# Kernel optimization log

Hardware: AMD Instinct MI355X
Metric: run time of the kernel (lower is better)

## Reference

```python
import jax, jax.numpy as jnp
import numpy as np

B, L, H, M, E, NH, R = 4, 512, 1024, 128, 64, 16, 1024   # docs, seq, hidden, mentions, entities, heads, pairs
D, BLK, C = 768, 64, 97                                   # embed_size, block_size, num_class


def setup_inputs() -> dict:
    key = jax.random.key(0)
    ks = jax.random.split(key, 9)
    seq_lhs = jax.random.normal(ks[0], (B, L, H), jnp.float32)
    ent_lhs = jax.random.normal(ks[1], (B, M, H), jnp.float32)
    ent_to_seq_attn = jax.random.uniform(ks[2], (B, NH, M, L), jnp.float32)
    entity_id_labels = jax.random.randint(ks[3], (B, M), 0, E, jnp.int32)
    hts = jax.random.randint(ks[4], (B, R, 2), 0, E, jnp.int32)
    Wh = jax.random.normal(ks[5], (2 * H, D), jnp.float32) * 0.02
    Wt = jax.random.normal(ks[6], (2 * H, D), jnp.float32) * 0.02
    Wb = jax.random.normal(ks[7], (D * BLK, C), jnp.float32) * 0.02
    return dict(seq_lhs=seq_lhs, ent_lhs=ent_lhs, ent_to_seq_attn=ent_to_seq_attn,
                entity_id_labels=entity_id_labels, hts=hts,
                Wh=Wh, bh=jnp.zeros((D,), jnp.float32),
                Wt=Wt, bt=jnp.zeros((D,), jnp.float32),
                Wb=Wb, bb=jnp.zeros((C,), jnp.float32))


def reference(seq_lhs, ent_lhs, ent_to_seq_attn, entity_id_labels, hts, Wh, bh, Wt, bt, Wb, bb):
    # --- hrt_pool: segment logsumexp / mean over mentions per entity ---
    mask = entity_id_labels[:, None, :] == jnp.arange(E, dtype=entity_id_labels.dtype)[None, :, None]  # [B,E,M]
    cnt = mask.sum(-1)  # [B,E]
    neg = jnp.asarray(-1e30, ent_lhs.dtype)
    masked = jnp.where(mask[..., None], ent_lhs[:, None, :, :], neg)          # [B,E,M,H]
    lse = jax.nn.logsumexp(masked, axis=2)                                    # [B,E,H]
    ent_emb = jnp.where((cnt > 0)[..., None], lse, 0.0)
    mf = mask.astype(ent_to_seq_attn.dtype)
    attn_sum = jnp.einsum('bem,bhml->behl', mf, ent_to_seq_attn)              # [B,E,NH,L]
    denom = jnp.maximum(cnt, 1).astype(attn_sum.dtype)[..., None, None]
    ent_attn = jnp.where((cnt > 0)[..., None, None], attn_sum / denom, 0.0)
    # --- gather head/tail entities per pair ---
    h_idx, t_idx = hts[..., 0], hts[..., 1]                                   # [B,R]
    hs = jnp.take_along_axis(ent_emb, h_idx[..., None], axis=1)               # [B,R,H]
    ts = jnp.take_along_axis(ent_emb, t_idx[..., None], axis=1)
    h_attn = jnp.take_along_axis(ent_attn, h_idx[..., None, None], axis=1)    # [B,R,NH,L]
    t_attn = jnp.take_along_axis(ent_attn, t_idx[..., None, None], axis=1)
    ht_attn = (h_attn * t_attn).mean(axis=2)                                  # [B,R,L]
    ht_attn = ht_attn / (ht_attn.sum(-1, keepdims=True) + 1e-5)
    rel = jnp.einsum('brl,bld->brd', ht_attn, seq_lhs)                        # [B,R,H]
    # --- extractors + block bilinear ---
    hcat = jnp.concatenate([hs, rel], -1).reshape(B * R, 2 * H)
    tcat = jnp.concatenate([ts, rel], -1).reshape(B * R, 2 * H)
    hv = jnp.tanh(hcat @ Wh + bh)
    tv = jnp.tanh(tcat @ Wt + bt)
    b1 = hv.reshape(-1, D // BLK, BLK)
    b2 = tv.reshape(-1, D // BLK, BLK)
    bl = (b1[:, :, :, None] * b2[:, :, None, :]).reshape(-1, D * BLK)
    return bl @ Wb + bb                                                       # [B*R, C]
```

## Files before the change

### kernel.cpp

```cpp
#include <hip/hip_runtime.h>
#include <hip/hip_bf16.h>
#include <math.h>

#define B_  4
#define L_  512
#define H_  1024
#define M_  128
#define E_  64
#define NH_ 16
#define R_  1024
#define D_  768
#define BLK_ 64
#define C_  97
#define NROW (B_*R_)
#define KB_  (D_/BLK_)

typedef __attribute__((ext_vector_type(8))) unsigned short ushort8;
typedef __attribute__((ext_vector_type(4))) unsigned short ushort4v;
typedef __attribute__((ext_vector_type(8))) short s8;
typedef __attribute__((ext_vector_type(4))) float f4;

__device__ __forceinline__ unsigned short f2bf(float x) {
    unsigned u = __builtin_bit_cast(unsigned, x);
    unsigned r = (u + 0x7fffu + ((u >> 16) & 1u)) >> 16;
    return (unsigned short)r;
}
__device__ __forceinline__ float bf2f(unsigned short h) {
    unsigned u = ((unsigned)h) << 16;
    return __builtin_bit_cast(float, u);
}
__device__ __forceinline__ float lo16f(unsigned u) { return __builtin_bit_cast(float, u << 16); }
__device__ __forceinline__ float hi16f(unsigned u) { return __builtin_bit_cast(float, u & 0xffff0000u); }

__device__ __forceinline__ void gload_lds16(const unsigned short* g, unsigned short* l)
{
    __builtin_amdgcn_global_load_lds(
        (const __attribute__((address_space(1))) unsigned int*)g,
        (__attribute__((address_space(3))) unsigned int*)l, 16, 0, 0);
}

__global__ __launch_bounds__(256) void pool_lse(
    const float* __restrict__ ent_lhs, const int* __restrict__ labels,
    unsigned short* __restrict__ ent_embB)
{
    int be = blockIdx.x, b = be >> 6, e = be & 63;
    __shared__ int midx[M_];
    __shared__ int scnt;
    if (threadIdx.x == 0) scnt = 0;
    __syncthreads();
    if (threadIdx.x < M_) {
        if (labels[b*M_ + threadIdx.x] == e) {
            int p = atomicAdd(&scnt, 1);
            midx[p] = threadIdx.x;
        }
    }
    __syncthreads();
    int cnt = scnt;
    for (int h = threadIdx.x; h < H_; h += blockDim.x) {
        float r = 0.f;
        if (cnt > 0) {
            const float* base = ent_lhs + (size_t)b*M_*H_ + h;
            float mx = -INFINITY;
            for (int k = 0; k < cnt; ++k) mx = fmaxf(mx, base[(size_t)midx[k]*H_]);
            float s = 0.f;
            for (int k = 0; k < cnt; ++k) s += expf(base[(size_t)midx[k]*H_] - mx);
            r = mx + logf(s);
        }
        ent_embB[(size_t)be*H_ + h] = f2bf(r);
    }
}

__global__ __launch_bounds__(256) void pool_attn(
    const float* __restrict__ attn, const int* __restrict__ labels,
    unsigned short* __restrict__ ent_attnB)
{
    int e  = blockIdx.x;
    int y  = blockIdx.y;
    int b  = y >> 4, nh = y & 15;
    __shared__ int midx[M_];
    __shared__ int scnt;
    if (threadIdx.x == 0) scnt = 0;
    __syncthreads();
    if (threadIdx.x < M_) {
        if (labels[b*M_ + threadIdx.x] == e) {
            int p = atomicAdd(&scnt, 1);
            midx[p] = threadIdx.x;
        }
    }
    __syncthreads();
    int cnt = scnt;
    float inv = (cnt > 0) ? 1.f/(float)cnt : 0.f;
    const float* base = attn + ((size_t)(b*NH_ + nh)*M_)*L_;
    #pragma unroll
    for (int q = 0; q < 2; ++q) {
        int l = threadIdx.x + q*256;
        float s = 0.f;
        for (int k = 0; k < cnt; ++k) s += base[(size_t)midx[k]*L_ + l];
        ent_attnB[((size_t)(b*E_ + e)*NH_ + nh)*L_ + l] = f2bf(s * inv);
    }
}

__global__ __launch_bounds__(256) void pair_attn_kernel(
    const unsigned short* __restrict__ entA, const int* __restrict__ hts,
    unsigned short* __restrict__ htA)
{
    int w  = threadIdx.x >> 6, ln = threadIdx.x & 63;
    int br = blockIdx.x*4 + w, b = br >> 10;
    int hi = hts[br*2 + 0], ti = hts[br*2 + 1];
    const unsigned* ph = (const unsigned*)(entA + ((size_t)(b*E_ + hi)*NH_)*L_);
    const unsigned* pt = (const unsigned*)(entA + ((size_t)(b*E_ + ti)*NH_)*L_);
    float v0[4] = {0.f, 0.f, 0.f, 0.f};
    float v1[4] = {0.f, 0.f, 0.f, 0.f};
    #pragma unroll
    for (int nh = 0; nh < NH_; ++nh) {
        #pragma unroll
        for (int c = 0; c < 4; ++c) {
            int l2 = ln + c*64;
            unsigned a = ph[nh*(L_/2) + l2], d = pt[nh*(L_/2) + l2];
            v0[c] += lo16f(a)*lo16f(d);
            v1[c] += hi16f(a)*hi16f(d);
        }
    }
    float part = 0.f;
    #pragma unroll
    for (int c = 0; c < 4; ++c) part += v0[c] + v1[c];
    #pragma unroll
    for (int off = 32; off > 0; off >>= 1) part += __shfl_xor(part, off, 64);
    float norm = 1.f / (part*(1.f/16.f) + 1e-5f);
    #pragma unroll
    for (int c = 0; c < 4; ++c) {
        unsigned short o0 = f2bf(v0[c]*(1.f/16.f)*norm);
        unsigned short o1 = f2bf(v1[c]*(1.f/16.f)*norm);
        *(unsigned*)(htA + (size_t)br*L_ + (size_t)(ln + c*64)*2) = ((unsigned)o1 << 16) | o0;
    }
}

__global__ __launch_bounds__(256) void transpose_cvt_seq(const float* __restrict__ in,
                                                         unsigned short* __restrict__ outp)
{
    int b = blockIdx.z;
    int h0 = blockIdx.x*32, l0 = blockIdx.y*32;
    __shared__ float tile[32][33];
    int tx = threadIdx.x & 31, ty = threadIdx.x >> 5;
    #pragma unroll
    for (int p = 0; p < 4; ++p)
        tile[ty + p*8][tx] = in[((size_t)b*L_ + l0 + ty + p*8)*H_ + h0 + tx];
    __syncthreads();
    #pragma unroll
    for (int p = 0; p < 4; ++p)
        outp[((size_t)b*H_ + h0 + ty + p*8)*L_ + l0 + tx] = f2bf(tile[tx][ty + p*8]);
}

__global__ __launch_bounds__(256) void transpose_cvt_W(const float* __restrict__ Wh,
                                                       const float* __restrict__ Wt,
                                                       unsigned short* __restrict__ WhT,
                                                       unsigned short* __restrict__ WtT)
{
    const float* in = blockIdx.z ? Wt : Wh;
    unsigned short* outp = blockIdx.z ? WtT : WhT;
    int n0 = blockIdx.x*32, k0 = blockIdx.y*32;
    __shared__ float tile[32][33];
    int tx = threadIdx.x & 31, ty = threadIdx.x >> 5;
    #pragma unroll
    for (int p = 0; p < 4; ++p)
        tile[ty + p*8][tx] = in[((size_t)(k0 + ty + p*8))*D_ + n0 + tx];
    __syncthreads();
    #pragma unroll
    for (int p = 0; p < 4; ++p) {
        int n = n0 + ty + p*8;
        outp[(size_t)n*2048 + k0 + tx] = f2bf(tile[tx][ty + p*8]);
    }
}

__global__ __launch_bounds__(256) void prep_gather(const unsigned short* __restrict__ entE,
                                                   const int* __restrict__ hts,
                                                   unsigned short* __restrict__ Ah,
                                                   unsigned short* __restrict__ At)
{
    int n = blockIdx.x, b = n >> 10;
    int m = threadIdx.x >> 7, off = (threadIdx.x & 127)*8;
    int idx = hts[n*2 + m];
    const unsigned short* src = entE + (size_t)(b*E_ + idx)*H_ + off;
    unsigned short* dst = (m ? At : Ah) + (size_t)n*2048 + off;
    *(ushort8*)dst = *(const ushort8*)src;
}

__global__ __launch_bounds__(256) void prep_WbT(const float* __restrict__ Wb,
                                                unsigned short* __restrict__ outp)
{
    int blk = blockIdx.x;
    __shared__ float sW[64*97];
    const float* src = Wb + (size_t)blk*64*97;
    for (int e = threadIdx.x; e < 64*97; e += 256) sW[e] = src[e];
    __syncthreads();
    unsigned short* dst = outp + (size_t)blk*128*64;
    for (int e = threadIdx.x; e < 128*64; e += 256) {
        int wcq = e >> 12;
        int ct  = (e >> 10) & 3;
        int j2  = (e >> 9) & 1;
        int qd  = (e >> 7) & 3;
        int lm  = (e >> 3) & 15;
        int t   = e & 7;
        int c   = wcq*64 + ct*16 + lm;
        int j   = j2*32 + qd*8 + t;
        dst[e] = (c < C_) ? f2bf(sW[j*97 + c]) : (unsigned short)0;
    }
}

__device__ __forceinline__ void gemm128_core(const unsigned short* __restrict__ A,
                                             const unsigned short* __restrict__ Bt,
                                             int K, int row0, int col0,
                                             f4 (&acc)[4][4])
{
    __shared__ __attribute__((aligned(16))) unsigned short As[128][32];
    __shared__ __attribute__((aligned(16))) unsigned short Bs[128][32];
    int tid = threadIdx.x;
    int wave = tid >> 6, lane = tid & 63;
    int wr = wave & 1, wc = wave >> 1;
    int lm = lane & 15, quad = lane >> 4;

    for (int k0 = 0; k0 < K; k0 += 32) {
        #pragma unroll
        for (int s = 0; s < 2; ++s) {
            int ch = tid + s*256;
            int row = ch >> 2, part = ch & 3;
            gload_lds16(A  + (size_t)(row0 + row)*K + k0 + part*8, &As[0][0] + ch*8);
            gload_lds16(Bt + (size_t)(col0 + row)*K + k0 + part*8, &Bs[0][0] + ch*8);
        }
        __syncthreads();
        s8 a[4], b[4];
        #pragma unroll
        for (int ti = 0; ti < 4; ++ti) a[ti] = *(const s8*)&As[wr*64 + ti*16 + lm][quad*8];
        #pragma unroll
        for (int tj = 0; tj < 4; ++tj) b[tj] = *(const s8*)&Bs[wc*64 + tj*16 + lm][quad*8];
        #pragma unroll
        for (int ti = 0; ti < 4; ++ti)
            #pragma unroll
            for (int tj = 0; tj < 4; ++tj)
                acc[ti][tj] = __builtin_amdgcn_mfma_f32_16x16x32_bf16(a[ti], b[tj], acc[ti][tj], 0, 0, 0);
        __syncthreads();
    }
}

__global__ __launch_bounds__(256) void gemm_rel_mfma(const unsigned short* __restrict__ htA,
                                                     const unsigned short* __restrict__ seqT,
                                                     unsigned short* __restrict__ Ah,
                                                     unsigned short* __restrict__ At)
{
    int z = blockIdx.z;
    const unsigned short* A  = htA  + (size_t)z*R_*L_;
    const unsigned short* Bt = seqT + (size_t)z*H_*L_;
    int row0 = blockIdx.y*128, col0 = blockIdx.x*128;
    f4 acc[4][4] = {};
    gemm128_core(A, Bt, L_, row0, col0, acc);
    int lane = threadIdx.x & 63, wave = threadIdx.x >> 6;
    int wr = wave & 1, wc = wave >> 1, lm = lane & 15, quad = lane >> 4;
    #pragma unroll
    for (int ti = 0; ti < 4; ++ti)
        #pragma unroll
        for (int tj = 0; tj < 4; ++tj)
            #pragma unroll
            for (int r = 0; r < 4; ++r) {
                int n   = z*R_ + row0 + wr*64 + ti*16 + quad*4 + r;
                int col = col0 + wc*64 + tj*16 + lm;
                unsigned short v = f2bf(acc[ti][tj][r]);
                Ah[(size_t)n*2048 + 1024 + col] = v;
                At[(size_t)n*2048 + 1024 + col] = v;
            }
}

__global__ __launch_bounds__(256) void gemm_ext_mfma(
    const unsigned short* __restrict__ Ah, const unsigned short* __restrict__ At,
    const unsigned short* __restrict__ WhT, const unsigned short* __restrict__ WtT,
    const float* __restrict__ bh, const float* __restrict__ bt,
    float* __restrict__ hv, float* __restrict__ tv)
{
    int z = blockIdx.z;
    const unsigned short* A  = z ? At  : Ah;
    const unsigned short* Bt = z ? WtT : WhT;
    const float* bias = z ? bt : bh;
    float* C = z ? tv : hv;
    int row0 = blockIdx.y*128, col0 = blockIdx.x*128;
    f4 acc[4][4] = {};
    gemm128_core(A, Bt, 2048, row0, col0, acc);
    int lane = threadIdx.x & 63, wave = threadIdx.x >> 6;
    int wr = wave & 1, wc = wave >> 1, lm = lane & 15, quad = lane >> 4;
    #pragma unroll
    for (int ti = 0; ti < 4; ++ti)
        #pragma unroll
        for (int tj = 0; tj < 4; ++tj)
            #pragma unroll
            for (int r = 0; r < 4; ++r) {
                int row = row0 + wr*64 + ti*16 + quad*4 + r;
                int col = col0 + wc*64 + tj*16 + lm;
                float x = acc[ti][tj][r] + bias[col];
                float e = __expf(2.f*x);
                C[(size_t)row*D_ + col] = 1.f - 2.f/(e + 1.f);
            }
}

__global__ void out_init(const float* __restrict__ bb, float* __restrict__ out)
{
    int i = blockIdx.x*256 + threadIdx.x;
    if (i < NROW*C_) out[i] = bb[i % C_];
}

__device__ __forceinline__ void loadB_frag(const unsigned short* __restrict__ bbase,
                                           int i, s8 (&dst)[4][2])
{
    #pragma unroll
    for (int ct = 0; ct < 4; ++ct) {
        dst[ct][0] = *(const s8*)(bbase + (size_t)i*8192 + ct*1024);
        dst[ct][1] = *(const s8*)(bbase + (size_t)i*8192 + ct*1024 + 512);
    }
}

__device__ __forceinline__ void compute_i4(const s8 (&bfr)[4][2],
                                           const float (&sh)[4],
                                           const float (&tvv)[4][2][8],
                                           f4 (&acc)[4][4])
{
    s8 afr[4][2];
    #pragma unroll
    for (int rt = 0; rt < 4; ++rt)
        #pragma unroll
        for (int j2 = 0; j2 < 2; ++j2) {
            union { unsigned u[4]; s8 v; } cv;
            #pragma unroll
            for (int t2 = 0; t2 < 4; ++t2) {
                float pe = sh[rt] * tvv[rt][j2][t2*2];
                float po = sh[rt] * tvv[rt][j2][t2*2 + 1];
                cv.u[t2] = __builtin_amdgcn_perm(__builtin_bit_cast(unsigned, po),
                                                 __builtin_bit_cast(unsigned, pe),
                                                 0x07060302u);
            }
            afr[rt][j2] = cv.v;
        }
    #pragma unroll
    for (int ct = 0; ct < 4; ++ct)
        #pragma unroll
        for (int rt = 0; rt < 4; ++rt) {
            acc[rt][ct] = __builtin_amdgcn_mfma_f32_16x16x32_bf16(afr[rt][0], bfr[ct][0], acc[rt][ct], 0, 0, 0);
            acc[rt][ct] = __builtin_amdgcn_mfma_f32_16x16x32_bf16(afr[rt][1], bfr[ct][1], acc[rt][ct], 0, 0, 0);
        }
}

__global__ __launch_bounds__(256) void final_mfma(
    const float* __restrict__ hv,
    const float* __restrict__ tv,
    const unsigned short* __restrict__ WbT,
    float* __restrict__ out)
{
    int kb   = blockIdx.x;
    int row0 = blockIdx.y * 128;
    __shared__ __attribute__((aligned(16))) unsigned short hS[128][72];
    __shared__ __attribute__((aligned(16))) unsigned short tS[128][72];

    int tid = threadIdx.x;
    for (int e = tid; e < 2048; e += 256) {
        int r = e >> 4, part = e & 15;
        float4 xh = *(const float4*)(hv + (size_t)(row0 + r)*D_ + kb*BLK_ + part*4);
        float4 xt = *(const float4*)(tv + (size_t)(row0 + r)*D_ + kb*BLK_ + part*4);
        ushort4v ph = { f2bf(xh.x), f2bf(xh.y), f2bf(xh.z), f2bf(xh.w) };
        ushort4v pt = { f2bf(xt.x), f2bf(xt.y), f2bf(xt.z), f2bf(xt.w) };
        *(ushort4v*)&hS[r][part*4] = ph;
        *(ushort4v*)&tS[r][part*4] = pt;
    }
    int wave = tid >> 6, lane = tid & 63;
    int wr = wave & 1, wc = wave >> 1;
    int lm = lane & 15, quad = lane >> 4;
    __syncthreads();

    float tvv[4][2][8];
    #pragma unroll
    for (int rt = 0; rt < 4; ++rt)
        #pragma unroll
        for (int j2 = 0; j2 < 2; ++j2) {
            int r = wr*64 + rt*16 + lm;
            ushort8 w = *(const ushort8*)&tS[r][j2*32 + quad*8];
            #pragma unroll
            for (int t = 0; t < 8; ++t) tvv[rt][j2][t] = bf2f(w[t]);
        }

    f4 acc[4][4] = {};
    const unsigned short* bbase = WbT + (size_t)kb*(64*128*64)
                                + (size_t)wc*4096 + ((size_t)quad*16 + lm)*8;

    s8 bufA[4][2], bufB[4][2];
    loadB_frag(bbase, 0, bufA);
    for (int i0 = 0; i0 < 64; i0 += 2) {
        loadB_frag(bbase, i0 + 1, bufB);
        {
            float sh[4];
            #pragma unroll
            for (int rt = 0; rt < 4; ++rt) sh[rt] = bf2f(hS[wr*64 + rt*16 + lm][i0]);
            compute_i4(bufA, sh, tvv, acc);
        }
        if (i0 < 62) loadB_frag(bbase, i0 + 2, bufA);
        {
            float sh[4];
            #pragma unroll
            for (int rt = 0; rt < 4; ++rt) sh[rt] = bf2f(hS[wr*64 + rt*16 + lm][i0 + 1]);
            compute_i4(bufB, sh, tvv, acc);
        }
    }

    #pragma unroll
    for (int rt = 0; rt < 4; ++rt)
        #pragma unroll
        for (int ct = 0; ct < 4; ++ct)
            #pragma unroll
            for (int r = 0; r < 4; ++r) {
                int row = row0 + wr*64 + rt*16 + quad*4 + r;
                int col = wc*64 + ct*16 + lm;
                if (col < C_) atomicAdd(out + (size_t)row*C_ + col, acc[rt][ct][r]);
            }
}

extern "C" void kernel_launch(void* const* d_in, const int* in_sizes, int n_in,
                              void* d_out, int out_size, void* d_ws, size_t ws_size,
                              hipStream_t stream)
{
    const float* seq_lhs = (const float*)d_in[0];
    const float* ent_lhs = (const float*)d_in[1];
    const float* attn    = (const float*)d_in[2];
    const int*   labels  = (const int*)d_in[3];
    const int*   hts     = (const int*)d_in[4];
    const float* Wh      = (const float*)d_in[5];
    const float* bh      = (const float*)d_in[6];
    const float* Wt      = (const float*)d_in[7];
    const float* bt      = (const float*)d_in[8];
    const float* Wb      = (const float*)d_in[9];
    const float* bb      = (const float*)d_in[10];
    float* out = (float*)d_out;

    float* wsf      = (float*)d_ws;
    float* hv       = wsf;
    float* tv       = hv + 3145728;
    unsigned short* ent_embB  = (unsigned short*)(tv + 3145728);
    unsigned short* ent_attnB = ent_embB  + 262144;
    unsigned short* htA       = ent_attnB + 2097152;
    unsigned short* seqT      = htA       + 2097152;
    unsigned short* WhT       = seqT      + 2097152;
    unsigned short* WtT       = WhT       + 1572864;
    unsigned short* Ah        = WtT       + 1572864;
    unsigned short* At        = Ah        + 8388608;
    unsigned short* WbT       = At        + 8388608;

    transpose_cvt_W<<<dim3(24, 64, 2), 256, 0, stream>>>(Wh, Wt, WhT, WtT);
    prep_WbT<<<KB_*64, 256, 0, stream>>>(Wb, WbT);
    transpose_cvt_seq<<<dim3(32, 16, B_), 256, 0, stream>>>(seq_lhs, seqT);

    pool_lse<<<B_*E_, 256, 0, stream>>>(ent_lhs, labels, ent_embB);
    pool_attn<<<dim3(E_, B_*NH_), 256, 0, stream>>>(attn, labels, ent_attnB);
    pair_attn_kernel<<<B_*R_/4, 256, 0, stream>>>(ent_attnB, hts, htA);
    gemm_rel_mfma<<<dim3(8, 8, B_), 256, 0, stream>>>(htA, seqT, Ah, At);
    prep_gather<<<NROW, 256, 0, stream>>>(ent_embB, hts, Ah, At);
    gemm_ext_mfma<<<dim3(6, 32, 2), 256, 0, stream>>>(Ah, At, WhT, WtT, bh, bt, hv, tv);
    out_init<<<(NROW*C_ + 255)/256, 256, 0, stream>>>(bb, out);
    final_mfma<<<dim3(KB_, NROW/128), 256, 0, stream>>>(hv, tv, WbT, out);
}
```

Before: 300.4 us.

## Precompute entity projections once and split extractor GEMM to skip gathered half

Splits the concatenated extractor GEMM algebraically. The entity-embedding half is now computed once per entity (256 rows, split-K with atomicAdd into bias-initialized buffers) rather than once per pair (4096 rows). The per-pair GEMM now only covers the rel half (K=1024), adding the gathered entity projection in the epilogue. This removes the prep_gather kernel, the duplicated rel writes into Ah/At, and half of the largest GEMM's FLOPs, at the cost of fp32 atomics and an extra small GEMM launch.

```diff
diff --git a/kernel.cpp b/kernel.cpp
--- a/kernel.cpp
+++ b/kernel.cpp
@@ -172,19 +172,6 @@
     }
 }
 
-__global__ __launch_bounds__(256) void prep_gather(const unsigned short* __restrict__ entE,
-                                                   const int* __restrict__ hts,
-                                                   unsigned short* __restrict__ Ah,
-                                                   unsigned short* __restrict__ At)
-{
-    int n = blockIdx.x, b = n >> 10;
-    int m = threadIdx.x >> 7, off = (threadIdx.x & 127)*8;
-    int idx = hts[n*2 + m];
-    const unsigned short* src = entE + (size_t)(b*E_ + idx)*H_ + off;
-    unsigned short* dst = (m ? At : Ah) + (size_t)n*2048 + off;
-    *(ushort8*)dst = *(const ushort8*)src;
-}
-
 __global__ __launch_bounds__(256) void prep_WbT(const float* __restrict__ Wb,
                                                 unsigned short* __restrict__ outp)
 {
@@ -207,8 +194,8 @@
     }
 }
 
-__device__ __forceinline__ void gemm128_core(const unsigned short* __restrict__ A,
-                                             const unsigned short* __restrict__ Bt,
+__device__ __forceinline__ void gemm128_core(const unsigned short* __restrict__ A, int lda,
+                                             const unsigned short* __restrict__ Bt, int ldb,
                                              int K, int row0, int col0,
                                              f4 (&acc)[4][4])
 {
@@ -224,8 +211,8 @@
         for (int s = 0; s < 2; ++s) {
             int ch = tid + s*256;
             int row = ch >> 2, part = ch & 3;
-            gload_lds16(A  + (size_t)(row0 + row)*K + k0 + part*8, &As[0][0] + ch*8);
-            gload_lds16(Bt + (size_t)(col0 + row)*K + k0 + part*8, &Bs[0][0] + ch*8);
+            gload_lds16(A  + (size_t)(row0 + row)*lda + k0 + part*8, &As[0][0] + ch*8);
+            gload_lds16(Bt + (size_t)(col0 + row)*ldb + k0 + part*8, &Bs[0][0] + ch*8);
         }
         __syncthreads();
         s8 a[4], b[4];
@@ -244,15 +231,14 @@
 
 __global__ __launch_bounds__(256) void gemm_rel_mfma(const unsigned short* __restrict__ htA,
                                                      const unsigned short* __restrict__ seqT,
-                                                     unsigned short* __restrict__ Ah,
-                                                     unsigned short* __restrict__ At)
+                                                     unsigned short* __restrict__ relB)
 {
     int z = blockIdx.z;
     const unsigned short* A  = htA  + (size_t)z*R_*L_;
     const unsigned short* Bt = seqT + (size_t)z*H_*L_;
     int row0 = blockIdx.y*128, col0 = blockIdx.x*128;
     f4 acc[4][4] = {};
-    gemm128_core(A, Bt, L_, row0, col0, acc);
+    gemm128_core(A, L_, Bt, L_, L_, row0, col0, acc);
     int lane = threadIdx.x & 63, wave = threadIdx.x >> 6;
     int wr = wave & 1, wc = wave >> 1, lm = lane & 15, quad = lane >> 4;
     #pragma unroll
@@ -263,26 +249,22 @@
             for (int r = 0; r < 4; ++r) {
                 int n   = z*R_ + row0 + wr*64 + ti*16 + quad*4 + r;
                 int col = col0 + wc*64 + tj*16 + lm;
-                unsigned short v = f2bf(acc[ti][tj][r]);
-                Ah[(size_t)n*2048 + 1024 + col] = v;
-                At[(size_t)n*2048 + 1024 + col] = v;
+                relB[(size_t)n*H_ + col] = f2bf(acc[ti][tj][r]);
             }
 }
 
-__global__ __launch_bounds__(256) void gemm_ext_mfma(
-    const unsigned short* __restrict__ Ah, const unsigned short* __restrict__ At,
+__global__ __launch_bounds__(256) void gemm_p_mfma(
+    const unsigned short* __restrict__ ent_embB,
     const unsigned short* __restrict__ WhT, const unsigned short* __restrict__ WtT,
-    const float* __restrict__ bh, const float* __restrict__ bt,
-    float* __restrict__ hv, float* __restrict__ tv)
+    float* __restrict__ Ph, float* __restrict__ Pt)
 {
     int z = blockIdx.z;
-    const unsigned short* A  = z ? At  : Ah;
     const unsigned short* Bt = z ? WtT : WhT;
-    const float* bias = z ? bt : bh;
-    float* C = z ? tv : hv;
-    int row0 = blockIdx.y*128, col0 = blockIdx.x*128;
+    float* P = z ? Pt : Ph;
+    int mt = blockIdx.y & 1, ks = blockIdx.y >> 1;
+    int row0 = mt*128, col0 = blockIdx.x*128;
     f4 acc[4][4] = {};
-    gemm128_core(A, Bt, 2048, row0, col0, acc);
+    gemm128_core(ent_embB + ks*256, H_, Bt + ks*256, 2048, 256, row0, col0, acc);
     int lane = threadIdx.x & 63, wave = threadIdx.x >> 6;
     int wr = wave & 1, wc = wave >> 1, lm = lane & 15, quad = lane >> 4;
     #pragma unroll
@@ -293,16 +275,55 @@
             for (int r = 0; r < 4; ++r) {
                 int row = row0 + wr*64 + ti*16 + quad*4 + r;
                 int col = col0 + wc*64 + tj*16 + lm;
-                float x = acc[ti][tj][r] + bias[col];
+                atomicAdd(P + (size_t)row*D_ + col, acc[ti][tj][r]);
+            }
+}
+
+__global__ __launch_bounds__(256) void gemm_ext_mfma(
+    const unsigned short* __restrict__ relB,
+    const unsigned short* __restrict__ WhT, const unsigned short* __restrict__ WtT,
+    const float* __restrict__ Ph, const float* __restrict__ Pt,
+    const int* __restrict__ hts,
+    float* __restrict__ hv, float* __restrict__ tv)
+{
+    int z = blockIdx.z;
+    const unsigned short* Bt = (z ? WtT : WhT) + 1024;
+    const float* P = z ? Pt : Ph;
+    float* Cv = z ? tv : hv;
+    int row0 = blockIdx.y*128, col0 = blockIdx.x*128;
+    f4 acc[4][4] = {};
+    gemm128_core(relB, H_, Bt, 2048, H_, row0, col0, acc);
+    int lane = threadIdx.x & 63, wave = threadIdx.x >> 6;
+    int wr = wave & 1, wc = wave >> 1, lm = lane & 15, quad = lane >> 4;
+    #pragma unroll
+    for (int ti = 0; ti < 4; ++ti)
+        #pragma unroll
+        for (int r = 0; r < 4; ++r) {
+            int row = row0 + wr*64 + ti*16 + quad*4 + r;
+            int b   = row >> 10;
+            int idx = hts[row*2 + z];
+            const float* prow = P + ((size_t)(b*E_ + idx))*D_;
+            #pragma unroll
+            for (int tj = 0; tj < 4; ++tj) {
+                int col = col0 + wc*64 + tj*16 + lm;
+                float x = acc[ti][tj][r] + prow[col];
                 float e = __expf(2.f*x);
-                C[(size_t)row*D_ + col] = 1.f - 2.f/(e + 1.f);
+                Cv[(size_t)row*D_ + col] = 1.f - 2.f/(e + 1.f);
             }
-}
-
-__global__ void out_init(const float* __restrict__ bb, float* __restrict__ out)
+        }
+}
+
+__global__ void out_init(const float* __restrict__ bb,
+                         const float* __restrict__ bh, const float* __restrict__ bt,
+                         float* __restrict__ out,
+                         float* __restrict__ Ph, float* __restrict__ Pt)
 {
     int i = blockIdx.x*256 + threadIdx.x;
     if (i < NROW*C_) out[i] = bb[i % C_];
+    if (i < 256*D_) {
+        Ph[i] = bh[i % D_];
+        Pt[i] = bt[i % D_];
+    }
 }
 
 __device__ __forceinline__ void loadB_frag(const unsigned short* __restrict__ bbase,
@@ -437,26 +458,27 @@
     float* wsf      = (float*)d_ws;
     float* hv       = wsf;
     float* tv       = hv + 3145728;
-    unsigned short* ent_embB  = (unsigned short*)(tv + 3145728);
+    float* Ph       = tv + 3145728;
+    float* Pt       = Ph + 196608;
+    unsigned short* ent_embB  = (unsigned short*)(Pt + 196608);
     unsigned short* ent_attnB = ent_embB  + 262144;
     unsigned short* htA       = ent_attnB + 2097152;
     unsigned short* seqT      = htA       + 2097152;
     unsigned short* WhT       = seqT      + 2097152;
     unsigned short* WtT       = WhT       + 1572864;
-    unsigned short* Ah        = WtT       + 1572864;
-    unsigned short* At        = Ah        + 8388608;
-    unsigned short* WbT       = At        + 8388608;
+    unsigned short* relB      = WtT       + 1572864;
+    unsigned short* WbT       = relB      + 4194304;
 
     transpose_cvt_W<<<dim3(24, 64, 2), 256, 0, stream>>>(Wh, Wt, WhT, WtT);
     prep_WbT<<<KB_*64, 256, 0, stream>>>(Wb, WbT);
     transpose_cvt_seq<<<dim3(32, 16, B_), 256, 0, stream>>>(seq_lhs, seqT);
 
     pool_lse<<<B_*E_, 256, 0, stream>>>(ent_lhs, labels, ent_embB);
+    out_init<<<(NROW*C_ + 255)/256, 256, 0, stream>>>(bb, bh, bt, out, Ph, Pt);
+    gemm_p_mfma<<<dim3(6, 8, 2), 256, 0, stream>>>(ent_embB, WhT, WtT, Ph, Pt);
     pool_attn<<<dim3(E_, B_*NH_), 256, 0, stream>>>(attn, labels, ent_attnB);
     pair_attn_kernel<<<B_*R_/4, 256, 0, stream>>>(ent_attnB, hts, htA);
-    gemm_rel_mfma<<<dim3(8, 8, B_), 256, 0, stream>>>(htA, seqT, Ah, At);
-    prep_gather<<<NROW, 256, 0, stream>>>(ent_embB, hts, Ah, At);
-    gemm_ext_mfma<<<dim3(6, 32, 2), 256, 0, stream>>>(Ah, At, WhT, WtT, bh, bt, hv, tv);
-    out_init<<<(NROW*C_ + 255)/256, 256, 0, stream>>>(bb, out);
+    gemm_rel_mfma<<<dim3(8, 8, B_), 256, 0, stream>>>(htA, seqT, relB);
+    gemm_ext_mfma<<<dim3(6, 32, 2), 256, 0, stream>>>(relB, WhT, WtT, Ph, Pt, hts, hv, tv);
     final_mfma<<<dim3(KB_, NROW/128), 256, 0, stream>>>(hv, tv, WbT, out);
 }
```

After: 281.8 us. 1.07x faster.
